# Performance work log

Measured on AMD Instinct MI355X. Metric: run time of the kernel, lower is better.

## Reference

```python
import jax, jax.numpy as jnp
import numpy as np

B, T, S, ENC_D = 128, 48, 256, 512
U1, U2, ATTN_U, OUT_D = 256, 256, 128, 1
EMB_D = U1  # embedding_dim = lstm_units_list[0]


def _glorot(key, shape):
    fan_in, fan_out = shape[0], shape[1]
    lim = np.sqrt(6.0 / (fan_in + fan_out)).astype(np.float32)
    return jax.random.uniform(key, shape, jnp.float32, -lim, lim)


def setup_inputs() -> dict:
    key = jax.random.key(0)
    ks = jax.random.split(key, 20)
    inp = {
        'x_decoder_input': jax.random.normal(ks[0], (B, T, 1), jnp.float32),
        'enc_state_h1': jax.random.normal(ks[1], (B, U1), jnp.float32),
        'enc_state_c1': jax.random.normal(ks[2], (B, U1), jnp.float32),
        'enc_state_h2': jax.random.normal(ks[3], (B, U2), jnp.float32),
        'enc_state_c2': jax.random.normal(ks[4], (B, U2), jnp.float32),
        'encoder_outputs': jax.random.normal(ks[5], (B, S, ENC_D), jnp.float32),
        # embedding Dense(EMB_D, relu) on 1-dim input
        'emb_W': _glorot(ks[6], (1, EMB_D)), 'emb_b': jnp.zeros((EMB_D,), jnp.float32),
        # Bahdanau attention
        'W1': _glorot(ks[7], (ENC_D, ATTN_U)), 'b1': jnp.zeros((ATTN_U,), jnp.float32),
        'W2': _glorot(ks[8], (U2, ATTN_U)), 'b2': jnp.zeros((ATTN_U,), jnp.float32),
        'V': _glorot(ks[9], (ATTN_U, 1)), 'bV': jnp.zeros((1,), jnp.float32),
        # LSTM1: input dim = EMB_D + ENC_D
        'Wx1': _glorot(ks[10], (EMB_D + ENC_D, 4 * U1)),
        'Wh1': _glorot(ks[11], (U1, 4 * U1)),
        'bl1': jnp.zeros((4 * U1,), jnp.float32),
        # LSTM2: input dim = U1
        'Wx2': _glorot(ks[12], (U1, 4 * U2)),
        'Wh2': _glorot(ks[13], (U2, 4 * U2)),
        'bl2': jnp.zeros((4 * U2,), jnp.float32),
        # output Dense
        'Wo': _glorot(ks[14], (U2, OUT_D)), 'bo': jnp.zeros((OUT_D,), jnp.float32),
    }
    return inp


def _lstm_cell(x, h, c, Wx, Wh, b):
    z = x @ Wx + h @ Wh + b                     # [B, 4U]
    i, f, g, o = jnp.split(z, 4, axis=-1)       # Keras gate order i,f,c,o
    i = jax.nn.sigmoid(i); f = jax.nn.sigmoid(f)
    g = jnp.tanh(g); o = jax.nn.sigmoid(o)
    c_new = f * c + i * g
    h_new = o * jnp.tanh(c_new)
    return h_new, c_new


def reference(x_decoder_input, enc_state_h1, enc_state_c1, enc_state_h2, enc_state_c2,
              encoder_outputs, emb_W, emb_b, W1, b1, W2, b2, V, bV,
              Wx1, Wh1, bl1, Wx2, Wh2, bl2, Wo, bo):
    # teacher-forcing (training=True) path: input at step t is x_decoder_input[:, t]
    keys = encoder_outputs @ W1 + b1            # [B, S, ATTN_U], hoisted (values are constant)

    def step(carry, x_t):
        h1, c1, h2, c2 = carry
        emb = jax.nn.relu(x_t @ emb_W + emb_b)                          # [B, EMB_D]
        q = h2 @ W2 + b2                                                # [B, ATTN_U]
        score = jnp.tanh(keys + q[:, None, :]) @ V + bV                 # [B, S, 1]
        attn = jax.nn.softmax(score, axis=1)
        ctx = jnp.sum(attn * encoder_outputs, axis=1)                   # [B, ENC_D]
        lstm_in = jnp.concatenate([emb, ctx], axis=-1)                  # [B, EMB_D+ENC_D]
        h1n, c1n = _lstm_cell(lstm_in, h1, c1, Wx1, Wh1, bl1)
        h2n, c2n = _lstm_cell(h1n, h2, c2, Wx2, Wh2, bl2)
        pred = h2n @ Wo + bo                                            # [B, OUT_D]
        return (h1n, c1n, h2n, c2n), pred

    xs = jnp.transpose(x_decoder_input, (1, 0, 2))                      # [T, B, 1]
    carry0 = (enc_state_h1, enc_state_c1, enc_state_h2, enc_state_c2)
    _, preds = jax.lax.scan(step, carry0, xs)                           # [T, B, OUT_D]
    return jnp.transpose(preds, (1, 0, 2))                              # [B, T, OUT_D]
```

## Files before the change

kernel.cpp:

```cpp
#include <hip/hip_runtime.h>
#include <hip/hip_fp16.h>

#define AGENT __HIP_MEMORY_SCOPE_AGENT

typedef _Float16 v8h __attribute__((ext_vector_type(8)));
typedef float    v4f __attribute__((ext_vector_type(4)));
typedef unsigned long long u64;

#define OFF_KEYSH  0UL
#define OFF_WBF    8388608UL
#define OFF_WCF    10485760UL
#define OFF_W1T    11534336UL
#define OFF_CTXU   11796480UL
#define OFF_SU     12320768UL
#define OFF_H1     12321792UL
#define OFF_H2     12452864UL
#define OFF_CNT    12583936UL
#define WS_CORE    12585984UL
#define OFF_ENCH   12585984UL
#define WS_FULL    46140416UL

static __device__ __forceinline__ float fast_tanh(float x){
    float e = __expf(2.0f*x);
    return 1.0f - 2.0f*__builtin_amdgcn_rcpf(e + 1.0f);
}
static __device__ __forceinline__ float fast_sigm(float x){
    return __builtin_amdgcn_rcpf(1.0f + __expf(-x));
}

static __device__ __forceinline__ void gbar(int* cnt, int idx){
    __builtin_amdgcn_s_waitcnt(0);
    __syncthreads();
    if(threadIdx.x == 0){
        int* sub = &cnt[256 + ((blockIdx.x >> 5) << 4)];
        int old = __hip_atomic_fetch_add(sub, 1, __ATOMIC_RELAXED, AGENT);
        if(old == 31){
            __hip_atomic_store(sub, 0, __ATOMIC_RELAXED, AGENT);
            __builtin_amdgcn_s_waitcnt(0);
            __hip_atomic_fetch_add(&cnt[idx], 1, __ATOMIC_RELAXED, AGENT);
        }
        while(__hip_atomic_load(&cnt[idx], __ATOMIC_RELAXED, AGENT) < 8)
            __builtin_amdgcn_s_sleep(1);
    }
    __syncthreads();
}

__global__ __launch_bounds__(256) void setup_kernel(
    const float* __restrict__ Wx1, const float* __restrict__ Wh1,
    const float* __restrict__ Wx2, const float* __restrict__ Wh2,
    const float* __restrict__ W1,
    const float* __restrict__ h1_in, const float* __restrict__ h2_in,
    const float* __restrict__ enc,
    __half* __restrict__ WbF, __half* __restrict__ WcF, float* __restrict__ W1t,
    unsigned int* __restrict__ h1d, unsigned int* __restrict__ h2d,
    int* __restrict__ cnt, __half* __restrict__ encH, long long total)
{
    long long id0 = (long long)blockIdx.x*blockDim.x + threadIdx.x;
    long long stride = (long long)gridDim.x*blockDim.x;
    for(long long id = id0; id < total; id += stride){
        if(id < 1048576LL){
            int j = (int)(id & 7), lane = (int)((id >> 3) & 63);
            int tile = (int)(id >> 9);
            int nt = tile & 63, kt = tile >> 6;
            int c = nt*16 + (lane & 15);
            int n = (c & 3)*256 + (c >> 2);
            int k = kt*32 + (lane >> 4)*8 + j;
            float v = (k < 768) ? Wx1[k*1024 + n] : Wh1[(k-768)*1024 + n];
            WbF[id] = __float2half(v);
        } else if(id < 1572864LL){
            long long i2 = id - 1048576LL;
            int j = (int)(i2 & 7), lane = (int)((i2 >> 3) & 63);
            int tile = (int)(i2 >> 9);
            int nt = tile & 63, kt = tile >> 6;
            int c = nt*16 + (lane & 15);
            int n = (c & 3)*256 + (c >> 2);
            int k = kt*32 + (lane >> 4)*8 + j;
            float v = (k < 256) ? Wx2[k*1024 + n] : Wh2[(k-256)*1024 + n];
            WcF[i2] = __float2half(v);
        } else if(id < 1638400LL){
            long long i3 = id - 1572864LL;
            int u = (int)(i3 >> 9), e = (int)(i3 & 511);
            W1t[i3] = W1[e*128 + u];
        } else if(id < 1654784LL){
            long long i4 = id - 1638400LL;
            int b = (int)(i4 >> 7), j = (int)(i4 & 127);
            __half2 p = __floats2half2_rn(h1_in[b*256 + 2*j], h1_in[b*256 + 2*j + 1]);
            h1d[i4] = __builtin_bit_cast(unsigned int, p);
        } else if(id < 1671168LL){
            long long i5 = id - 1654784LL;
            int b = (int)(i5 >> 7), j = (int)(i5 & 127);
            __half2 p = __floats2half2_rn(h2_in[b*256 + 2*j], h2_in[b*256 + 2*j + 1]);
            h2d[i5] = __builtin_bit_cast(unsigned int, p);
        } else if(id < 1671680LL){
            cnt[(int)(id - 1671168LL)] = 0;
        } else {
            long long i6 = id - 1671680LL;
            encH[i6] = __float2half(enc[i6]);
        }
    }
}

__global__ __launch_bounds__(256) void keys_kernel(
    const float* __restrict__ enc, const float* __restrict__ W1t,
    const float* __restrict__ b1, __half* __restrict__ keysH)
{
    const int bb = blockIdx.x;
    const int b  = bb >> 3, sq = bb & 7;
    const int tid = threadIdx.x;
    const int u = tid & 127, sh = tid >> 7;
    const int s0 = sq*32 + sh*16;
    float acc[16];
    #pragma unroll
    for(int i = 0; i < 16; ++i) acc[i] = 0.0f;
    const float* wp = W1t + (size_t)u*512;
    const float* xp = enc + (size_t)(b*256 + s0)*512;
    for(int e = 0; e < 512; e += 4){
        float4 wv = *(const float4*)(wp + e);
        #pragma unroll
        for(int i = 0; i < 16; ++i){
            float4 xv = *(const float4*)(xp + (size_t)i*512 + e);
            acc[i] += wv.x*xv.x + wv.y*xv.y + wv.z*xv.z + wv.w*xv.w;
        }
    }
    const float bu = b1[u];
    __half* op = keysH + (size_t)(b*128 + u)*256 + s0;
    #pragma unroll
    for(int i = 0; i < 16; ++i) op[i] = __float2half(acc[i] + bu);
}

__global__ __launch_bounds__(1024) void decoder_v6(
    const float* __restrict__ xdec, const float* __restrict__ embW, const float* __restrict__ embb,
    const float* __restrict__ W2, const float* __restrict__ b2,
    const float* __restrict__ V, const float* __restrict__ bVp,
    const float* __restrict__ Wo, const float* __restrict__ bop,
    const float* __restrict__ bl1, const float* __restrict__ bl2,
    const float* __restrict__ c1_in, const float* __restrict__ c2_in,
    const float* __restrict__ enc, const __half* __restrict__ encH,
    const __half* __restrict__ keysH,
    const __half* __restrict__ WbF, const __half* __restrict__ WcF,
    float* CTXU, float* SU,
    unsigned int* h1d, unsigned int* h2d,
    int* cnt, float* __restrict__ out, int useEncH)
{
    const int tid  = threadIdx.x;
    const int bid  = blockIdx.x;
    const int ab   = bid >> 1, sh = bid & 1;
    const int NT   = bid >> 2, Hq = bid & 3;
    const int w    = tid >> 6;
    const int lane = tid & 63;
    const int cl   = lane & 15;
    const int kg   = lane >> 4;
    const int g    = w >> 3;
    const int wk   = w & 7;
    const int uu   = lane >> 4;
    const int bl   = lane & 15;

    __shared__ __align__(16) float zb[2][8][16][20];
    __shared__ float spb[8][128];
    __shared__ float qv[128];
    __shared__ float pexpA[128];
    __shared__ float h2s[256];
    __shared__ float red[16];
    __shared__ float Vs[128];
    __shared__ float embWs[256];
    __shared__ float embbs[256];

    float b2r = 0.0f; float2 wo2 = make_float2(0.f, 0.f);
    if(tid < 128){
        Vs[tid] = V[tid]; b2r = b2[tid];
        wo2 = make_float2(Wo[2*tid], Wo[2*tid+1]);
    }
    if(tid < 256){ embWs[tid] = embW[tid]; embbs[tid] = embb[tid]; }
    const float bVv = bVp[0], bov = bop[0];

    uint4 wfb[4];
    #pragma unroll
    for(int i = 0; i < 4; ++i){
        int kt = wk*4 + i;
        wfb[i] = *(const uint4*)((const char*)WbF + (((size_t)(kt*64 + NT)*64 + lane) << 4));
    }
    uint4 wfc[2];
    #pragma unroll
    for(int i = 0; i < 2; ++i){
        int kt = wk*2 + i;
        wfc[i] = *(const uint4*)((const char*)WcF + (((size_t)(kt*64 + NT)*64 + lane) << 4));
    }

    const int ug = 4*NT + uu;
    float bi1=0,bf1=0,bg1=0,bo1=0,bi2=0,bf2=0,bg2=0,bo2=0;
    float c1r = 0.0f, c2r = 0.0f;
    if(wk == 0){
        bi1 = bl1[ug]; bf1 = bl1[256+ug]; bg1 = bl1[512+ug]; bo1 = bl1[768+ug];
        bi2 = bl2[ug]; bf2 = bl2[256+ug]; bg2 = bl2[512+ug]; bo2 = bl2[768+ug];
        const int bb0 = 32*Hq + 16*g + bl;
        c1r = c1_in[bb0*256 + ug];
        c2r = c2_in[bb0*256 + ug];
    }
    __syncthreads();

    for(int t = 0; t < 48; ++t){
        const int rpar = t & 1, wpar = rpar ^ 1;
        unsigned int* h1r = h1d + rpar*16384;
        unsigned int* h1w = h1d + wpar*16384;
        unsigned int* h2r = h2d + rpar*16384;
        unsigned int* h2w = h2d + wpar*16384;

        if(tid < 128){
            unsigned int v = __hip_atomic_load(&h2r[ab*128 + tid], __ATOMIC_RELAXED, AGENT);
            float2 f = __half22float2(__builtin_bit_cast(__half2, v));
            h2s[2*tid] = f.x; h2s[2*tid+1] = f.y;
            float pv = f.x*wo2.x + f.y*wo2.y;
            #pragma unroll
            for(int off = 32; off >= 1; off >>= 1) pv += __shfl_xor(pv, off);
            if(lane == 0) red[8 + w] = pv;
        }
        __syncthreads();
        if(tid == 0 && t > 0 && sh == 0) out[ab*48 + (t-1)] = red[8] + red[9] + bov;
        {
            const int u = tid & 127, kq = tid >> 7, k0 = kq*32;
            float a = 0.0f;
            #pragma unroll 8
            for(int k = k0; k < k0 + 32; ++k) a += h2s[k]*W2[k*128 + u];
            spb[kq][u] = a;
        }
        __syncthreads();
        if(tid < 128){
            float a = b2r;
            #pragma unroll
            for(int j = 0; j < 8; ++j) a += spb[j][tid];
            qv[tid] = a;
        }
        __syncthreads();
        {
            const int sl = tid & 127, uo = tid >> 7;
            const __half* kp = keysH + ((size_t)(ab*128 + uo*16))*256 + sh*128 + sl;
            float a = 0.0f;
            #pragma unroll 8
            for(int ui = 0; ui < 16; ++ui){
                const int u = uo*16 + ui;
                a += fast_tanh(__half2float(kp[(size_t)ui*256]) + qv[u]) * Vs[u];
            }
            spb[uo][sl] = a;
        }
        __syncthreads();
        if(tid < 128){
            float sc = bVv;
            #pragma unroll
            for(int j = 0; j < 8; ++j) sc += spb[j][tid];
            float p = __expf(sc);
            pexpA[tid] = p;
            float su = p;
            #pragma unroll
            for(int off = 32; off >= 1; off >>= 1) su += __shfl_xor(su, off);
            if(lane == 0) red[w] = su;
        }
        __syncthreads();
        if(tid == 0)
            __hip_atomic_store(&SU[ab*2 + sh], red[0] + red[1], __ATOMIC_RELAXED, AGENT);
        if(tid < 512){
            float a = 0.0f;
            if(useEncH){
                const __half* ep = encH + ((size_t)(ab*256 + sh*128))*512 + tid;
                #pragma unroll 8
                for(int s = 0; s < 128; ++s) a += pexpA[s]*__half2float(ep[(size_t)s*512]);
            } else {
                const float* ep = enc + ((size_t)(ab*256 + sh*128))*512 + tid;
                #pragma unroll 8
                for(int s = 0; s < 128; ++s) a += pexpA[s]*ep[(size_t)s*512];
            }
            __hip_atomic_store(&CTXU[((size_t)ab*2 + sh)*512 + tid], a, __ATOMIC_RELAXED, AGENT);
        }
        gbar(cnt, 3*t + 0);

        {
            const int rowB = 32*Hq + 16*g + cl;
            uint4 af[4];
            if(wk < 2){
                const float x = xdec[rowB*48 + t];
                #pragma unroll
                for(int i = 0; i < 4; ++i){
                    const int K = wk*128 + 32*i + kg*8;
                    v8h hv;
                    #pragma unroll
                    for(int j = 0; j < 8; ++j)
                        hv[j] = (_Float16)fmaxf(x*embWs[K+j] + embbs[K+j], 0.0f);
                    af[i] = __builtin_bit_cast(uint4, hv);
                }
            } else if(wk < 6){
                u64 sv = __hip_atomic_load((u64*)(SU + rowB*2), __ATOMIC_RELAXED, AGENT);
                float2 ss = __builtin_bit_cast(float2, sv);
                float rn = 1.0f/(ss.x + ss.y);
                u64* cp = (u64*)(CTXU + (size_t)rowB*1024);
                #pragma unroll
                for(int i = 0; i < 4; ++i){
                    const int e0 = (wk-2)*128 + 32*i + kg*8;
                    u64 a0 = __hip_atomic_load(cp + (e0>>1),       __ATOMIC_RELAXED, AGENT);
                    u64 a1 = __hip_atomic_load(cp + (e0>>1) + 1,   __ATOMIC_RELAXED, AGENT);
                    u64 a2 = __hip_atomic_load(cp + (e0>>1) + 2,   __ATOMIC_RELAXED, AGENT);
                    u64 a3 = __hip_atomic_load(cp + (e0>>1) + 3,   __ATOMIC_RELAXED, AGENT);
                    u64 b0 = __hip_atomic_load(cp + 256 + (e0>>1),     __ATOMIC_RELAXED, AGENT);
                    u64 b1 = __hip_atomic_load(cp + 256 + (e0>>1) + 1, __ATOMIC_RELAXED, AGENT);
                    u64 b2v= __hip_atomic_load(cp + 256 + (e0>>1) + 2, __ATOMIC_RELAXED, AGENT);
                    u64 b3 = __hip_atomic_load(cp + 256 + (e0>>1) + 3, __ATOMIC_RELAXED, AGENT);
                    float2 fa0 = __builtin_bit_cast(float2, a0), fb0 = __builtin_bit_cast(float2, b0);
                    float2 fa1 = __builtin_bit_cast(float2, a1), fb1 = __builtin_bit_cast(float2, b1);
                    float2 fa2 = __builtin_bit_cast(float2, a2), fb2 = __builtin_bit_cast(float2, b2v);
                    float2 fa3 = __builtin_bit_cast(float2, a3), fb3 = __builtin_bit_cast(float2, b3);
                    v8h hv;
                    hv[0] = (_Float16)((fa0.x+fb0.x)*rn); hv[1] = (_Float16)((fa0.y+fb0.y)*rn);
                    hv[2] = (_Float16)((fa1.x+fb1.x)*rn); hv[3] = (_Float16)((fa1.y+fb1.y)*rn);
                    hv[4] = (_Float16)((fa2.x+fb2.x)*rn); hv[5] = (_Float16)((fa2.y+fb2.y)*rn);
                    hv[6] = (_Float16)((fa3.x+fb3.x)*rn); hv[7] = (_Float16)((fa3.y+fb3.y)*rn);
                    af[i] = __builtin_bit_cast(uint4, hv);
                }
            } else {
                const u64* hp = (const u64*)h1r + (size_t)rowB*64;
                #pragma unroll
                for(int i = 0; i < 4; ++i){
                    const int K0 = (wk-6)*128 + 32*i + kg*8;
                    u64 q0 = __hip_atomic_load((u64*)hp + (K0>>2),     __ATOMIC_RELAXED, AGENT);
                    u64 q1 = __hip_atomic_load((u64*)hp + (K0>>2) + 1, __ATOMIC_RELAXED, AGENT);
                    af[i] = make_uint4((unsigned int)q0, (unsigned int)(q0>>32),
                                       (unsigned int)q1, (unsigned int)(q1>>32));
                }
            }
            v4f acc = {0.0f, 0.0f, 0.0f, 0.0f};
            #pragma unroll
            for(int i = 0; i < 4; ++i)
                acc = __builtin_amdgcn_mfma_f32_16x16x32_f16(
                        __builtin_bit_cast(v8h, af[i]), __builtin_bit_cast(v8h, wfb[i]), acc, 0, 0, 0);
            #pragma unroll
            for(int r = 0; r < 4; ++r) zb[g][wk][kg*4 + r][cl] = acc[r];
            __syncthreads();
            if(wk == 0){
                v4f z = {0.0f, 0.0f, 0.0f, 0.0f};
                #pragma unroll
                for(int q = 0; q < 8; ++q) z += *(const v4f*)&zb[g][q][bl][uu*4];
                float cn = fast_sigm(z.y + bf1)*c1r + fast_sigm(z.x + bi1)*fast_tanh(z.z + bg1);
                c1r = cn;
                float hn = fast_sigm(z.w + bo1)*fast_tanh(cn);
                float hp2 = __shfl_xor(hn, 16);
                if((uu & 1) == 0){
                    __half2 ph = __floats2half2_rn(hn, hp2);
                    int bb = 32*Hq + 16*g + bl;
                    __hip_atomic_store(&h1w[bb*128 + 2*NT + (uu >> 1)],
                                       __builtin_bit_cast(unsigned int, ph),
                                       __ATOMIC_RELAXED, AGENT);
                }
            }
        }
        gbar(cnt, 3*t + 1);

        {
            const int rowB = 32*Hq + 16*g + cl;
            uint4 af2[2];
            #pragma unroll
            for(int i = 0; i < 2; ++i){
                const int kt = wk*2 + i;
                const int K0 = kt*32 + kg*8;
                const u64* hp = (kt < 8) ? ((const u64*)h1w + (size_t)rowB*64 + (K0>>2))
                                         : ((const u64*)h2r + (size_t)rowB*64 + ((K0-256)>>2));
                u64 q0 = __hip_atomic_load((u64*)hp,     __ATOMIC_RELAXED, AGENT);
                u64 q1 = __hip_atomic_load((u64*)hp + 1, __ATOMIC_RELAXED, AGENT);
                af2[i] = make_uint4((unsigned int)q0, (unsigned int)(q0>>32),
                                    (unsigned int)q1, (unsigned int)(q1>>32));
            }
            v4f acc = {0.0f, 0.0f, 0.0f, 0.0f};
            #pragma unroll
            for(int i = 0; i < 2; ++i)
                acc = __builtin_amdgcn_mfma_f32_16x16x32_f16(
                        __builtin_bit_cast(v8h, af2[i]), __builtin_bit_cast(v8h, wfc[i]), acc, 0, 0, 0);
            #pragma unroll
            for(int r = 0; r < 4; ++r) zb[g][wk][kg*4 + r][cl] = acc[r];
            __syncthreads();
            if(wk == 0){
                v4f z = {0.0f, 0.0f, 0.0f, 0.0f};
                #pragma unroll
                for(int q = 0; q < 8; ++q) z += *(const v4f*)&zb[g][q][bl][uu*4];
                float cn = fast_sigm(z.y + bf2)*c2r + fast_sigm(z.x + bi2)*fast_tanh(z.z + bg2);
                c2r = cn;
                float hn = fast_sigm(z.w + bo2)*fast_tanh(cn);
                float hp2 = __shfl_xor(hn, 16);
                if((uu & 1) == 0){
                    __half2 ph = __floats2half2_rn(hn, hp2);
                    int bb = 32*Hq + 16*g + bl;
                    __hip_atomic_store(&h2w[bb*128 + 2*NT + (uu >> 1)],
                                       __builtin_bit_cast(unsigned int, ph),
                                       __ATOMIC_RELAXED, AGENT);
                }
            }
        }
        gbar(cnt, 3*t + 2);
    }

    if((bid & 1) == 0){
        if(tid < 128){
            unsigned int v = __hip_atomic_load(&h2d[ab*128 + tid], __ATOMIC_RELAXED, AGENT);
            float2 f = __half22float2(__builtin_bit_cast(__half2, v));
            float pv = f.x*wo2.x + f.y*wo2.y;
            #pragma unroll
            for(int off = 32; off >= 1; off >>= 1) pv += __shfl_xor(pv, off);
            if(lane == 0) red[w] = pv;
        }
        __syncthreads();
        if(tid == 0) out[ab*48 + 47] = red[0] + red[1] + bov;
    }
}

extern "C" void kernel_launch(void* const* d_in, const int* in_sizes, int n_in,
                              void* d_out, int out_size, void* d_ws, size_t ws_size,
                              hipStream_t stream)
{
    const float* xdec = (const float*)d_in[0];
    const float* h1_in= (const float*)d_in[1];
    const float* c1_in= (const float*)d_in[2];
    const float* h2_in= (const float*)d_in[3];
    const float* c2_in= (const float*)d_in[4];
    const float* enc  = (const float*)d_in[5];
    const float* embW = (const float*)d_in[6];
    const float* embb = (const float*)d_in[7];
    const float* W1   = (const float*)d_in[8];
    const float* b1   = (const float*)d_in[9];
    const float* W2   = (const float*)d_in[10];
    const float* b2   = (const float*)d_in[11];
    const float* V    = (const float*)d_in[12];
    const float* bV   = (const float*)d_in[13];
    const float* Wx1  = (const float*)d_in[14];
    const float* Wh1  = (const float*)d_in[15];
    const float* bl1  = (const float*)d_in[16];
    const float* Wx2  = (const float*)d_in[17];
    const float* Wh2  = (const float*)d_in[18];
    const float* bl2  = (const float*)d_in[19];
    const float* Wo   = (const float*)d_in[20];
    const float* bo   = (const float*)d_in[21];

    if(ws_size < WS_CORE) return;

    char* ws = (char*)d_ws;
    __half* keysH = (__half*)(ws + OFF_KEYSH);
    __half* WbF   = (__half*)(ws + OFF_WBF);
    __half* WcF   = (__half*)(ws + OFF_WCF);
    float*  W1t   = (float*) (ws + OFF_W1T);
    float*  CTXU  = (float*) (ws + OFF_CTXU);
    float*  SU    = (float*) (ws + OFF_SU);
    unsigned int* h1d = (unsigned int*)(ws + OFF_H1);
    unsigned int* h2d = (unsigned int*)(ws + OFF_H2);
    int*    cnt   = (int*)   (ws + OFF_CNT);
    __half* encH  = (__half*)(ws + OFF_ENCH);

    const int useEncH = (ws_size >= WS_FULL) ? 1 : 0;
    const long long total = useEncH ? 18448896LL : 1671680LL;

    hipLaunchKernelGGL(setup_kernel, dim3(4096), dim3(256), 0, stream,
        Wx1, Wh1, Wx2, Wh2, W1, h1_in, h2_in, enc,
        WbF, WcF, W1t, h1d, h2d, cnt, encH, total);

    hipLaunchKernelGGL(keys_kernel, dim3(1024), dim3(256), 0, stream,
        enc, W1t, b1, keysH);

    hipLaunchKernelGGL(decoder_v6, dim3(256), dim3(1024), 0, stream,
        xdec, embW, embb, W2, b2, V, bV, Wo, bo, bl1, bl2,
        c1_in, c2_in, enc, encH, keysH, WbF, WcF, CTXU, SU,
        h1d, h2d, cnt, (float*)d_out, useEncH);
}
```

Measured before the change: 2.153 ms.

## Split grid barrier into four independent batch groups and parallelize context reduction

Blocks are remapped so each group of 64 blocks owns 32 batch rows and all 64 N-tiles. That makes the recurrence independent per group, so the grid-wide barrier becomes a per-group barrier over 64 blocks instead of 256. The context sum now uses all 1024 threads, each handling a quarter of the sequence with half2 loads, and the partials are reduced through shared memory. The aim is lower barrier latency per timestep and faster attention context, at the cost of an extra shared buffer and a syncthreads, and each group's blocks now read the full weight set.

```diff
diff --git a/kernel.cpp b/kernel.cpp
--- a/kernel.cpp
+++ b/kernel.cpp
@@ -16,9 +16,9 @@
 #define OFF_H1     12321792UL
 #define OFF_H2     12452864UL
 #define OFF_CNT    12583936UL
-#define WS_CORE    12585984UL
-#define OFF_ENCH   12585984UL
-#define WS_FULL    46140416UL
+#define WS_CORE    12588032UL
+#define OFF_ENCH   12588032UL
+#define WS_FULL    46142464UL
 
 static __device__ __forceinline__ float fast_tanh(float x){
     float e = __expf(2.0f*x);
@@ -28,18 +28,19 @@
     return __builtin_amdgcn_rcpf(1.0f + __expf(-x));
 }
 
-static __device__ __forceinline__ void gbar(int* cnt, int idx){
+static __device__ __forceinline__ void gbar(int* cnt, int grp, int idx){
     __builtin_amdgcn_s_waitcnt(0);
     __syncthreads();
     if(threadIdx.x == 0){
-        int* sub = &cnt[256 + ((blockIdx.x >> 5) << 4)];
+        int* base = cnt + (grp << 8);
+        int* sub  = base + 160 + (((blockIdx.x >> 5) & 1) << 4);
         int old = __hip_atomic_fetch_add(sub, 1, __ATOMIC_RELAXED, AGENT);
         if(old == 31){
             __hip_atomic_store(sub, 0, __ATOMIC_RELAXED, AGENT);
             __builtin_amdgcn_s_waitcnt(0);
-            __hip_atomic_fetch_add(&cnt[idx], 1, __ATOMIC_RELAXED, AGENT);
-        }
-        while(__hip_atomic_load(&cnt[idx], __ATOMIC_RELAXED, AGENT) < 8)
+            __hip_atomic_fetch_add(&base[idx], 1, __ATOMIC_RELAXED, AGENT);
+        }
+        while(__hip_atomic_load(&base[idx], __ATOMIC_RELAXED, AGENT) < 2)
             __builtin_amdgcn_s_sleep(1);
     }
     __syncthreads();
@@ -91,10 +92,10 @@
             int b = (int)(i5 >> 7), j = (int)(i5 & 127);
             __half2 p = __floats2half2_rn(h2_in[b*256 + 2*j], h2_in[b*256 + 2*j + 1]);
             h2d[i5] = __builtin_bit_cast(unsigned int, p);
-        } else if(id < 1671680LL){
+        } else if(id < 1672192LL){
             cnt[(int)(id - 1671168LL)] = 0;
         } else {
-            long long i6 = id - 1671680LL;
+            long long i6 = id - 1672192LL;
             encH[i6] = __float2half(enc[i6]);
         }
     }
@@ -128,7 +129,7 @@
     for(int i = 0; i < 16; ++i) op[i] = __float2half(acc[i] + bu);
 }
 
-__global__ __launch_bounds__(1024) void decoder_v6(
+__global__ __launch_bounds__(1024) void decoder_v8(
     const float* __restrict__ xdec, const float* __restrict__ embW, const float* __restrict__ embb,
     const float* __restrict__ W2, const float* __restrict__ b2,
     const float* __restrict__ V, const float* __restrict__ bVp,
@@ -144,8 +145,12 @@
 {
     const int tid  = threadIdx.x;
     const int bid  = blockIdx.x;
-    const int ab   = bid >> 1, sh = bid & 1;
-    const int NT   = bid >> 2, Hq = bid & 3;
+    const int gq   = bid >> 6;
+    const int j    = bid & 63;
+    const int ab   = 32*gq + (j >> 1);
+    const int sh   = j & 1;
+    const int NT   = j;
+    const int R0   = 32*gq;
     const int w    = tid >> 6;
     const int lane = tid & 63;
     const int cl   = lane & 15;
@@ -164,6 +169,7 @@
     __shared__ float Vs[128];
     __shared__ float embWs[256];
     __shared__ float embbs[256];
+    __shared__ __align__(16) float ctxp[4][512];
 
     float b2r = 0.0f; float2 wo2 = make_float2(0.f, 0.f);
     if(tid < 128){
@@ -192,7 +198,7 @@
     if(wk == 0){
         bi1 = bl1[ug]; bf1 = bl1[256+ug]; bg1 = bl1[512+ug]; bo1 = bl1[768+ug];
         bi2 = bl2[ug]; bf2 = bl2[256+ug]; bg2 = bl2[512+ug]; bo2 = bl2[768+ug];
-        const int bb0 = 32*Hq + 16*g + bl;
+        const int bb0 = R0 + 16*g + bl;
         c1r = c1_in[bb0*256 + ug];
         c2r = c2_in[bb0*256 + ug];
     }
@@ -227,7 +233,7 @@
         if(tid < 128){
             float a = b2r;
             #pragma unroll
-            for(int j = 0; j < 8; ++j) a += spb[j][tid];
+            for(int j2 = 0; j2 < 8; ++j2) a += spb[j2][tid];
             qv[tid] = a;
         }
         __syncthreads();
@@ -246,7 +252,7 @@
         if(tid < 128){
             float sc = bVv;
             #pragma unroll
-            for(int j = 0; j < 8; ++j) sc += spb[j][tid];
+            for(int j2 = 0; j2 < 8; ++j2) sc += spb[j2][tid];
             float p = __expf(sc);
             pexpA[tid] = p;
             float su = p;
@@ -257,23 +263,38 @@
         __syncthreads();
         if(tid == 0)
             __hip_atomic_store(&SU[ab*2 + sh], red[0] + red[1], __ATOMIC_RELAXED, AGENT);
+        {
+            const int e2 = tid & 255, s4 = tid >> 8;
+            float a0 = 0.0f, a1 = 0.0f;
+            if(useEncH){
+                const __half2* ep = (const __half2*)(encH
+                    + ((size_t)(ab*256 + sh*128 + s4*32))*512 + 2*e2);
+                #pragma unroll 8
+                for(int si = 0; si < 32; ++si){
+                    float att = pexpA[s4*32 + si];
+                    float2 ev = __half22float2(ep[(size_t)si*256]);
+                    a0 += att*ev.x; a1 += att*ev.y;
+                }
+            } else {
+                const float* ep = enc + ((size_t)(ab*256 + sh*128 + s4*32))*512 + 2*e2;
+                #pragma unroll 8
+                for(int si = 0; si < 32; ++si){
+                    float att = pexpA[s4*32 + si];
+                    float2 ev = *(const float2*)(ep + (size_t)si*512);
+                    a0 += att*ev.x; a1 += att*ev.y;
+                }
+            }
+            *(float2*)&ctxp[s4][2*e2] = make_float2(a0, a1);
+        }
+        __syncthreads();
         if(tid < 512){
-            float a = 0.0f;
-            if(useEncH){
-                const __half* ep = encH + ((size_t)(ab*256 + sh*128))*512 + tid;
-                #pragma unroll 8
-                for(int s = 0; s < 128; ++s) a += pexpA[s]*__half2float(ep[(size_t)s*512]);
-            } else {
-                const float* ep = enc + ((size_t)(ab*256 + sh*128))*512 + tid;
-                #pragma unroll 8
-                for(int s = 0; s < 128; ++s) a += pexpA[s]*ep[(size_t)s*512];
-            }
+            float a = ctxp[0][tid] + ctxp[1][tid] + ctxp[2][tid] + ctxp[3][tid];
             __hip_atomic_store(&CTXU[((size_t)ab*2 + sh)*512 + tid], a, __ATOMIC_RELAXED, AGENT);
         }
-        gbar(cnt, 3*t + 0);
+        gbar(cnt, gq, 3*t + 0);
 
         {
-            const int rowB = 32*Hq + 16*g + cl;
+            const int rowB = R0 + 16*g + cl;
             uint4 af[4];
             if(wk < 2){
                 const float x = xdec[rowB*48 + t];
@@ -282,8 +303,8 @@
                     const int K = wk*128 + 32*i + kg*8;
                     v8h hv;
                     #pragma unroll
-                    for(int j = 0; j < 8; ++j)
-                        hv[j] = (_Float16)fmaxf(x*embWs[K+j] + embbs[K+j], 0.0f);
+                    for(int j2 = 0; j2 < 8; ++j2)
+                        hv[j2] = (_Float16)fmaxf(x*embWs[K+j2] + embbs[K+j2], 0.0f);
                     af[i] = __builtin_bit_cast(uint4, hv);
                 }
             } else if(wk < 6){
@@ -342,17 +363,17 @@
                 float hp2 = __shfl_xor(hn, 16);
                 if((uu & 1) == 0){
                     __half2 ph = __floats2half2_rn(hn, hp2);
-                    int bb = 32*Hq + 16*g + bl;
+                    int bb = R0 + 16*g + bl;
                     __hip_atomic_store(&h1w[bb*128 + 2*NT + (uu >> 1)],
                                        __builtin_bit_cast(unsigned int, ph),
                                        __ATOMIC_RELAXED, AGENT);
                 }
             }
         }
-        gbar(cnt, 3*t + 1);
+        gbar(cnt, gq, 3*t + 1);
 
         {
-            const int rowB = 32*Hq + 16*g + cl;
+            const int rowB = R0 + 16*g + cl;
             uint4 af2[2];
             #pragma unroll
             for(int i = 0; i < 2; ++i){
@@ -383,17 +404,17 @@
                 float hp2 = __shfl_xor(hn, 16);
                 if((uu & 1) == 0){
                     __half2 ph = __floats2half2_rn(hn, hp2);
-                    int bb = 32*Hq + 16*g + bl;
+                    int bb = R0 + 16*g + bl;
                     __hip_atomic_store(&h2w[bb*128 + 2*NT + (uu >> 1)],
                                        __builtin_bit_cast(unsigned int, ph),
                                        __ATOMIC_RELAXED, AGENT);
                 }
             }
         }
-        gbar(cnt, 3*t + 2);
-    }
-
-    if((bid & 1) == 0){
+        gbar(cnt, gq, 3*t + 2);
+    }
+
+    if(sh == 0){
         if(tid < 128){
             unsigned int v = __hip_atomic_load(&h2d[ab*128 + tid], __ATOMIC_RELAXED, AGENT);
             float2 f = __half22float2(__builtin_bit_cast(__half2, v));
@@ -449,7 +470,7 @@
     __half* encH  = (__half*)(ws + OFF_ENCH);
 
     const int useEncH = (ws_size >= WS_FULL) ? 1 : 0;
-    const long long total = useEncH ? 18448896LL : 1671680LL;
+    const long long total = useEncH ? 18449408LL : 1672192LL;
 
     hipLaunchKernelGGL(setup_kernel, dim3(4096), dim3(256), 0, stream,
         Wx1, Wh1, Wx2, Wh2, W1, h1_in, h2_in, enc,
@@ -458,7 +479,7 @@
     hipLaunchKernelGGL(keys_kernel, dim3(1024), dim3(256), 0, stream,
         enc, W1t, b1, keysH);
 
-    hipLaunchKernelGGL(decoder_v6, dim3(256), dim3(1024), 0, stream,
+    hipLaunchKernelGGL(decoder_v8, dim3(256), dim3(1024), 0, stream,
         xdec, embW, embb, W2, b2, V, bV, Wo, bo, bl1, bl2,
         c1_in, c2_in, enc, encH, keysH, WbF, WcF, CTXU, SU,
         h1d, h2d, cnt, (float*)d_out, useEncH);
```

New measurement: 2.158 ms. About the same (+0.2%).
